# Performance work log

Measured on AMD Instinct MI355X. Metric: run time of the kernel, lower is better.

## Reference

```python
import jax, jax.numpy as jnp
import numpy as np

MARGIN = 0.2
MAX_VIOLATION = False
REDUCTION = 'mean'

N, D = 8192, 512


def setup_inputs() -> dict:
    key = jax.random.key(0)
    k1, k2, k3 = jax.random.split(key, 3)
    im = jax.random.normal(k1, (N, D), dtype=jnp.float32)
    s = jax.random.normal(k2, (N, D), dtype=jnp.float32)
    ex_s = jax.random.normal(k3, (N, D), dtype=jnp.float32)
    return {"im": im, "s": s, "ex_s": ex_s}


def l2_sim(im, s):
    # scores[i, j] = -||im_i - s_j||_2, computed via the GEMM identity
    # ||a-b||^2 = ||a||^2 + ||b||^2 - 2 a.b (same math, no NxNxD intermediate)
    im_sq = jnp.sum(im * im, axis=1)            # [N_im]
    s_sq = jnp.sum(s * s, axis=1)               # [N_s]
    d2 = im_sq[:, None] + s_sq[None, :] - 2.0 * (im @ s.T)  # [N_im, N_s]
    return -jnp.sqrt(jnp.maximum(d2, 0.0))


def reference(im, s, ex_s):
    scores = l2_sim(im, ex_s)        # [N_im, N_ex]
    scores_orig = l2_sim(im, s)      # [N_im, N_im]
    diagonal = jnp.diagonal(scores_orig)[:, None]            # [N_im, 1]
    cost_s = jnp.maximum(MARGIN + scores - diagonal, 0.0)    # [N_im, N_ex]
    if MAX_VIOLATION:
        cost_s = jnp.max(cost_s, axis=1)
    if REDUCTION == 'mean':
        return jnp.mean(cost_s)
    return jnp.sum(cost_s)
```

## Files before the change

kernel.cpp:

```cpp
#include <hip/hip_runtime.h>
#include <hip/hip_bf16.h>

#define NROW 8192
#define DDIM 512
#define MARGIN 0.2f

typedef __bf16 bf16x8 __attribute__((ext_vector_type(8)));
typedef float f32x4 __attribute__((ext_vector_type(4)));

__device__ __forceinline__ void gload16(const void* g, void* l) {
    __builtin_amdgcn_global_load_lds(
        (const __attribute__((address_space(1))) void*)g,
        (__attribute__((address_space(3))) void*)l, 16, 0, 0);
}

#define BAR() __builtin_amdgcn_s_barrier()

__global__ __launch_bounds__(256) void prep_kernel(
    const float* __restrict__ im, const float* __restrict__ s,
    const float* __restrict__ ex,
    ushort* __restrict__ Abf, ushort* __restrict__ Bbf,
    float2* __restrict__ idat, float* __restrict__ exsq) {
    int b = blockIdx.x;
    bool isim = b < NROW;
    int row = isim ? b : b - NROW;
    const float* src = isim ? im : ex;
    ushort* dst = isim ? Abf : Bbf;
    int tid = threadIdx.x;

    float2 v = ((const float2*)(src + (size_t)row * DDIM))[tid];
    __hip_bfloat16 hx = __float2bfloat16(v.x);
    __hip_bfloat16 hy = __float2bfloat16(v.y);
    unsigned packed = (unsigned)*(const ushort*)&hx | ((unsigned)*(const ushort*)&hy << 16);
    ((unsigned*)(dst + (size_t)row * DDIM))[tid] = packed;

    float ssq = v.x * v.x + v.y * v.y;
    float dsq = 0.f;
    if (isim) {
        float2 sv = ((const float2*)(s + (size_t)row * DDIM))[tid];
        float dx = v.x - sv.x, dy = v.y - sv.y;
        dsq = dx * dx + dy * dy;
    }
    #pragma unroll
    for (int off = 32; off > 0; off >>= 1) {
        ssq += __shfl_down(ssq, off);
        dsq += __shfl_down(dsq, off);
    }
    __shared__ float sred[8];
    int lane = tid & 63, w = tid >> 6;
    if (lane == 0) { sred[w] = ssq; sred[4 + w] = dsq; }
    __syncthreads();
    if (tid == 0) {
        float S = sred[0] + sred[1] + sred[2] + sred[3];
        float Dd = sred[4] + sred[5] + sred[6] + sred[7];
        if (isim) idat[row] = make_float2(S, MARGIN + sqrtf(Dd));
        else      exsq[row] = S;
    }
}

__global__ __launch_bounds__(256, 2) void gemm_cost_kernel(
    const ushort* __restrict__ Abf, const ushort* __restrict__ Bbf,
    const float2* __restrict__ idat, const float* __restrict__ exsq,
    float* __restrict__ partials) {
    __shared__ __align__(16) ushort sA[2][8192];
    __shared__ __align__(16) ushort sB[2][8192];
    __shared__ float redbuf[4];

    int bid0 = blockIdx.x;
    int c = bid0 & 7;
    int sq = bid0 >> 3;
    int win = sq >> 6;
    int pos = sq & 63;
    int bi = c * 8 + (pos & 7);
    int bj = win * 8 + (pos >> 3);
    int bid = bi * 64 + bj;
    int ibase = bi * 128, jbase = bj * 128;
    int tid = threadIdx.x, lane = tid & 63, w = tid >> 6;
    int wr = w >> 1, wc = w & 1;

    int r = tid >> 3;
    int pc = tid & 7;
    int lc = pc ^ (r & 7);
    const ushort* aG = Abf + (size_t)(ibase + r) * DDIM + lc * 8;
    const ushort* bG = Bbf + (size_t)(jbase + r) * DDIM + lc * 8;
    ushort* aL = &sA[0][0] + r * 64 + pc * 8;
    ushort* bL = &sB[0][0] + r * 64 + pc * 8;

    auto STAGE = [&](int h) {
        if (h >= 32) return;
        int kt = h >> 2, q = h & 3;
        if (q < 2) {
            const ushort* g = aG + q * (64 * DDIM) + kt * 64;
            ushort* l = aL + (kt & 1) * 8192 + q * 4096;
            gload16(g, l);
            gload16(g + 32 * DDIM, l + 2048);
        } else {
            int qq = q - 2;
            const ushort* g = bG + qq * (64 * DDIM) + kt * 64;
            ushort* l = bL + (kt & 1) * 8192 + qq * 4096;
            gload16(g, l);
            gload16(g + 32 * DDIM, l + 2048);
        }
    };

    int l15 = lane & 15;
    int pc0 = (((lane >> 4) ^ (lane & 7)) * 8);
    int pc1 = pc0 ^ 32;
    int aoff = (wr * 64 + l15) * 64;
    int boff = (wc * 64 + l15) * 64;

    f32x4 acc[4][4] = {};

    STAGE(0); STAGE(1); STAGE(2); STAGE(3);
    STAGE(4); STAGE(5); STAGE(6); STAGE(7);
    asm volatile("s_waitcnt vmcnt(8)" ::: "memory");
    BAR();

    #pragma unroll
    for (int t = 0; t < 8; ++t) {
        const ushort* pA = &sA[t & 1][0];
        const ushort* pB = &sB[t & 1][0];
        bf16x8 a[4][2], b[4][2];

        #pragma unroll
        for (int m = 0; m < 4; ++m) {
            a[m][0] = *(const bf16x8*)(pA + aoff + m * 1024 + pc0);
            a[m][1] = *(const bf16x8*)(pA + aoff + m * 1024 + pc1);
        }
        #pragma unroll
        for (int n = 0; n < 4; ++n) {
            b[n][0] = *(const bf16x8*)(pB + boff + n * 1024 + pc0);
            b[n][1] = *(const bf16x8*)(pB + boff + n * 1024 + pc1);
        }
        __builtin_amdgcn_s_setprio(1);
        #pragma unroll
        for (int m = 0; m < 4; ++m)
            #pragma unroll
            for (int n = 0; n < 4; ++n) {
                acc[m][n] = __builtin_amdgcn_mfma_f32_16x16x32_bf16(a[m][0], b[n][0], acc[m][n], 0, 0, 0);
                acc[m][n] = __builtin_amdgcn_mfma_f32_16x16x32_bf16(a[m][1], b[n][1], acc[m][n], 0, 0, 0);
            }
        __builtin_amdgcn_s_setprio(0);

        BAR();
        STAGE(4 * (t + 2) + 0); STAGE(4 * (t + 2) + 1);
        STAGE(4 * (t + 2) + 2); STAGE(4 * (t + 2) + 3);
        if (t < 6)       asm volatile("s_waitcnt vmcnt(8)" ::: "memory");
        else if (t == 6) asm volatile("s_waitcnt vmcnt(0)" ::: "memory");
        BAR();
    }

    float jt[4];
    #pragma unroll
    for (int n = 0; n < 4; ++n) jt[n] = exsq[jbase + wc * 64 + n * 16 + l15];
    int r0 = (lane >> 4) * 4;
    float lsum = 0.f;
    #pragma unroll
    for (int m = 0; m < 4; ++m) {
        #pragma unroll
        for (int rg = 0; rg < 4; ++rg) {
            int i = ibase + wr * 64 + m * 16 + r0 + rg;
            float2 id = idat[i];
            #pragma unroll
            for (int n = 0; n < 4; ++n) {
                float d2 = fmaxf(id.x + jt[n] - 2.0f * acc[m][n][rg], 0.0f);
                lsum += fmaxf(id.y - sqrtf(d2), 0.0f);
            }
        }
    }
    #pragma unroll
    for (int off = 32; off > 0; off >>= 1) lsum += __shfl_down(lsum, off);
    if (lane == 0) redbuf[w] = lsum;
    __syncthreads();
    if (tid == 0) partials[bid] = redbuf[0] + redbuf[1] + redbuf[2] + redbuf[3];
}

__global__ __launch_bounds__(256) void finalize_kernel(
    const float* __restrict__ partials, float* __restrict__ out) {
    float acc = 0.f;
    for (int t = threadIdx.x; t < 4096; t += 256) acc += partials[t];
    #pragma unroll
    for (int off = 32; off > 0; off >>= 1) acc += __shfl_down(acc, off);
    __shared__ float sred[4];
    int lane = threadIdx.x & 63, w = threadIdx.x >> 6;
    if (lane == 0) sred[w] = acc;
    __syncthreads();
    if (threadIdx.x == 0) {
        float total = sred[0] + sred[1] + sred[2] + sred[3];
        out[0] = total * (1.0f / (8192.0f * 8192.0f));
    }
}

extern "C" void kernel_launch(void* const* d_in, const int* in_sizes, int n_in,
                              void* d_out, int out_size, void* d_ws, size_t ws_size,
                              hipStream_t stream) {
    const float* im = (const float*)d_in[0];
    const float* s  = (const float*)d_in[1];
    const float* ex = (const float*)d_in[2];

    char* ws = (char*)d_ws;
    ushort* Abf   = (ushort*)(ws);
    ushort* Bbf   = (ushort*)(ws + 8388608);
    float2* idat  = (float2*)(ws + 16777216);
    float*  exsq  = (float*)(ws + 16842752);
    float*  parts = (float*)(ws + 16875520);

    prep_kernel<<<2 * NROW, 256, 0, stream>>>(im, s, ex, Abf, Bbf, idat, exsq);
    gemm_cost_kernel<<<(NROW / 128) * (NROW / 128), 256, 0, stream>>>(Abf, Bbf, idat, exsq, parts);
    finalize_kernel<<<1, 256, 0, stream>>>(parts, (float*)d_out);
}
```

Measured before the change: 111.4 us.

## Load B operand directly from global into registers, bypassing LDS

Removes the shared-memory staging buffer for the B (ex_s) tile. Each wave now reads its MFMA B fragments straight from global memory into double-buffered registers, prefetching the next k-step after the current MFMAs. This halves LDS usage and removes the LDS reads for B. In exchange it adds vector registers, duplicates B loads across the two wave rows that share a column, and uses narrower, less coalesced global accesses whose latency is waited on inside each iteration.

```diff
diff --git a/kernel.cpp b/kernel.cpp
--- a/kernel.cpp
+++ b/kernel.cpp
@@ -63,7 +63,6 @@
     const float2* __restrict__ idat, const float* __restrict__ exsq,
     float* __restrict__ partials) {
     __shared__ __align__(16) ushort sA[2][8192];
-    __shared__ __align__(16) ushort sB[2][8192];
     __shared__ float redbuf[4];
 
     int bid0 = blockIdx.x;
@@ -82,71 +81,72 @@
     int pc = tid & 7;
     int lc = pc ^ (r & 7);
     const ushort* aG = Abf + (size_t)(ibase + r) * DDIM + lc * 8;
-    const ushort* bG = Bbf + (size_t)(jbase + r) * DDIM + lc * 8;
     ushort* aL = &sA[0][0] + r * 64 + pc * 8;
-    ushort* bL = &sB[0][0] + r * 64 + pc * 8;
 
     auto STAGE = [&](int h) {
-        if (h >= 32) return;
-        int kt = h >> 2, q = h & 3;
-        if (q < 2) {
-            const ushort* g = aG + q * (64 * DDIM) + kt * 64;
-            ushort* l = aL + (kt & 1) * 8192 + q * 4096;
-            gload16(g, l);
-            gload16(g + 32 * DDIM, l + 2048);
-        } else {
-            int qq = q - 2;
-            const ushort* g = bG + qq * (64 * DDIM) + kt * 64;
-            ushort* l = bL + (kt & 1) * 8192 + qq * 4096;
-            gload16(g, l);
-            gload16(g + 32 * DDIM, l + 2048);
-        }
+        if (h >= 16) return;
+        int kt = h >> 1, q = h & 1;
+        const ushort* g = aG + q * (64 * DDIM) + kt * 64;
+        ushort* l = aL + (kt & 1) * 8192 + q * 4096;
+        gload16(g, l);
+        gload16(g + 32 * DDIM, l + 2048);
     };
 
     int l15 = lane & 15;
     int pc0 = (((lane >> 4) ^ (lane & 7)) * 8);
     int pc1 = pc0 ^ 32;
     int aoff = (wr * 64 + l15) * 64;
-    int boff = (wc * 64 + l15) * 64;
+
+    const ushort* bG = Bbf + (size_t)(jbase + wc * 64 + l15) * DDIM + (lane >> 4) * 8;
+
+    bf16x8 bA[4][2], bB[4][2];
+    auto LOADB = [&](int t, bf16x8 (&b)[4][2]) {
+        if (t >= 8) return;
+        #pragma unroll
+        for (int n = 0; n < 4; ++n)
+            #pragma unroll
+            for (int ks = 0; ks < 2; ++ks)
+                b[n][ks] = *(const bf16x8*)(bG + (size_t)n * 16 * DDIM + t * 64 + ks * 32);
+    };
 
     f32x4 acc[4][4] = {};
 
-    STAGE(0); STAGE(1); STAGE(2); STAGE(3);
-    STAGE(4); STAGE(5); STAGE(6); STAGE(7);
-    asm volatile("s_waitcnt vmcnt(8)" ::: "memory");
+    STAGE(0); STAGE(1);
+    LOADB(0, bA);
+    STAGE(2); STAGE(3);
+    asm volatile("s_waitcnt vmcnt(4)" ::: "memory");
+    __builtin_amdgcn_sched_barrier(0);
     BAR();
 
     #pragma unroll
     for (int t = 0; t < 8; ++t) {
         const ushort* pA = &sA[t & 1][0];
-        const ushort* pB = &sB[t & 1][0];
-        bf16x8 a[4][2], b[4][2];
+        bf16x8 (&bcur)[4][2] = (t & 1) ? bB : bA;
+        bf16x8 (&bnxt)[4][2] = (t & 1) ? bA : bB;
+        bf16x8 a[4][2];
 
         #pragma unroll
         for (int m = 0; m < 4; ++m) {
             a[m][0] = *(const bf16x8*)(pA + aoff + m * 1024 + pc0);
             a[m][1] = *(const bf16x8*)(pA + aoff + m * 1024 + pc1);
         }
-        #pragma unroll
-        for (int n = 0; n < 4; ++n) {
-            b[n][0] = *(const bf16x8*)(pB + boff + n * 1024 + pc0);
-            b[n][1] = *(const bf16x8*)(pB + boff + n * 1024 + pc1);
-        }
         __builtin_amdgcn_s_setprio(1);
         #pragma unroll
         for (int m = 0; m < 4; ++m)
             #pragma unroll
             for (int n = 0; n < 4; ++n) {
-                acc[m][n] = __builtin_amdgcn_mfma_f32_16x16x32_bf16(a[m][0], b[n][0], acc[m][n], 0, 0, 0);
-                acc[m][n] = __builtin_amdgcn_mfma_f32_16x16x32_bf16(a[m][1], b[n][1], acc[m][n], 0, 0, 0);
+                acc[m][n] = __builtin_amdgcn_mfma_f32_16x16x32_bf16(a[m][0], bcur[n][0], acc[m][n], 0, 0, 0);
+                acc[m][n] = __builtin_amdgcn_mfma_f32_16x16x32_bf16(a[m][1], bcur[n][1], acc[m][n], 0, 0, 0);
             }
         __builtin_amdgcn_s_setprio(0);
+        LOADB(t + 1, bnxt);
 
         BAR();
-        STAGE(4 * (t + 2) + 0); STAGE(4 * (t + 2) + 1);
-        STAGE(4 * (t + 2) + 2); STAGE(4 * (t + 2) + 3);
-        if (t < 6)       asm volatile("s_waitcnt vmcnt(8)" ::: "memory");
+        STAGE(2 * (t + 2));
+        STAGE(2 * (t + 2) + 1);
+        if (t < 6)       asm volatile("s_waitcnt vmcnt(4)" ::: "memory");
         else if (t == 6) asm volatile("s_waitcnt vmcnt(0)" ::: "memory");
+        __builtin_amdgcn_sched_barrier(0);
         BAR();
     }
 
```

Result: slower. 189.7 us (+70.2%).

## Triple-buffer LDS stages and prefetch next-tile fragments into registers

Applied to the files above, without the earlier changes.

The GEMM mainloop moves from a double-buffered LDS ring to a three-stage ring that holds A and B together, so global loads are issued two k-tiles ahead. It also double-buffers the register fragments: LDS reads for the next k-tile are issued before the current tile's MFMAs, so LDS latency can hide behind matrix math. The larger LDS footprint (about 96KB) and extra registers force launch bounds down to one block per SIMD group, which lowers occupancy and the latency hiding that comes from running other blocks.

```diff
diff --git a/kernel.cpp b/kernel.cpp
--- a/kernel.cpp
+++ b/kernel.cpp
@@ -58,12 +58,11 @@
     }
 }
 
-__global__ __launch_bounds__(256, 2) void gemm_cost_kernel(
+__global__ __launch_bounds__(256, 1) void gemm_cost_kernel(
     const ushort* __restrict__ Abf, const ushort* __restrict__ Bbf,
     const float2* __restrict__ idat, const float* __restrict__ exsq,
     float* __restrict__ partials) {
-    __shared__ __align__(16) ushort sA[2][8192];
-    __shared__ __align__(16) ushort sB[2][8192];
+    __shared__ __align__(16) ushort sAB[3][16384];
     __shared__ float redbuf[4];
 
     int bid0 = blockIdx.x;
@@ -83,70 +82,84 @@
     int lc = pc ^ (r & 7);
     const ushort* aG = Abf + (size_t)(ibase + r) * DDIM + lc * 8;
     const ushort* bG = Bbf + (size_t)(jbase + r) * DDIM + lc * 8;
-    ushort* aL = &sA[0][0] + r * 64 + pc * 8;
-    ushort* bL = &sB[0][0] + r * 64 + pc * 8;
-
-    auto STAGE = [&](int h) {
-        if (h >= 32) return;
-        int kt = h >> 2, q = h & 3;
-        if (q < 2) {
-            const ushort* g = aG + q * (64 * DDIM) + kt * 64;
-            ushort* l = aL + (kt & 1) * 8192 + q * 4096;
-            gload16(g, l);
-            gload16(g + 32 * DDIM, l + 2048);
-        } else {
-            int qq = q - 2;
-            const ushort* g = bG + qq * (64 * DDIM) + kt * 64;
-            ushort* l = bL + (kt & 1) * 8192 + qq * 4096;
-            gload16(g, l);
-            gload16(g + 32 * DDIM, l + 2048);
-        }
+    ushort* lL = &sAB[0][0] + r * 64 + pc * 8;
+
+    auto STAGE = [&](int kt) {
+        if (kt >= 8) return;
+        ushort* base = lL + (kt % 3) * 16384;
+        const ushort* ga = aG + kt * 64;
+        const ushort* gb = bG + kt * 64;
+        #pragma unroll
+        for (int q = 0; q < 4; ++q)
+            gload16(ga + q * (32 * DDIM), base + q * 2048);
+        #pragma unroll
+        for (int q = 0; q < 4; ++q)
+            gload16(gb + q * (32 * DDIM), base + 8192 + q * 2048);
     };
 
     int l15 = lane & 15;
     int pc0 = (((lane >> 4) ^ (lane & 7)) * 8);
     int pc1 = pc0 ^ 32;
     int aoff = (wr * 64 + l15) * 64;
-    int boff = (wc * 64 + l15) * 64;
+    int boff = 8192 + (wc * 64 + l15) * 64;
 
     f32x4 acc[4][4] = {};
-
-    STAGE(0); STAGE(1); STAGE(2); STAGE(3);
-    STAGE(4); STAGE(5); STAGE(6); STAGE(7);
+    bf16x8 aR0[4][2], aR1[4][2], bR0[4][2], bR1[4][2];
+
+    STAGE(0); STAGE(1); STAGE(2);
     asm volatile("s_waitcnt vmcnt(8)" ::: "memory");
+    __builtin_amdgcn_sched_barrier(0);
     BAR();
+    {
+        const ushort* p0 = &sAB[0][0];
+        #pragma unroll
+        for (int m = 0; m < 4; ++m) {
+            aR0[m][0] = *(const bf16x8*)(p0 + aoff + m * 1024 + pc0);
+            aR0[m][1] = *(const bf16x8*)(p0 + aoff + m * 1024 + pc1);
+        }
+        #pragma unroll
+        for (int n = 0; n < 4; ++n) {
+            bR0[n][0] = *(const bf16x8*)(p0 + boff + n * 1024 + pc0);
+            bR0[n][1] = *(const bf16x8*)(p0 + boff + n * 1024 + pc1);
+        }
+    }
 
     #pragma unroll
     for (int t = 0; t < 8; ++t) {
-        const ushort* pA = &sA[t & 1][0];
-        const ushort* pB = &sB[t & 1][0];
-        bf16x8 a[4][2], b[4][2];
-
-        #pragma unroll
-        for (int m = 0; m < 4; ++m) {
-            a[m][0] = *(const bf16x8*)(pA + aoff + m * 1024 + pc0);
-            a[m][1] = *(const bf16x8*)(pA + aoff + m * 1024 + pc1);
-        }
-        #pragma unroll
-        for (int n = 0; n < 4; ++n) {
-            b[n][0] = *(const bf16x8*)(pB + boff + n * 1024 + pc0);
-            b[n][1] = *(const bf16x8*)(pB + boff + n * 1024 + pc1);
-        }
+        bf16x8 (&ac)[4][2] = (t & 1) ? aR1 : aR0;
+        bf16x8 (&bc)[4][2] = (t & 1) ? bR1 : bR0;
+        bf16x8 (&an)[4][2] = (t & 1) ? aR0 : aR1;
+        bf16x8 (&bn)[4][2] = (t & 1) ? bR0 : bR1;
+
+        if (t < 7) {
+            const ushort* pN = &sAB[0][0] + ((t + 1) % 3) * 16384;
+            #pragma unroll
+            for (int m = 0; m < 4; ++m) {
+                an[m][0] = *(const bf16x8*)(pN + aoff + m * 1024 + pc0);
+                an[m][1] = *(const bf16x8*)(pN + aoff + m * 1024 + pc1);
+            }
+            #pragma unroll
+            for (int n = 0; n < 4; ++n) {
+                bn[n][0] = *(const bf16x8*)(pN + boff + n * 1024 + pc0);
+                bn[n][1] = *(const bf16x8*)(pN + boff + n * 1024 + pc1);
+            }
+        }
+
         __builtin_amdgcn_s_setprio(1);
         #pragma unroll
         for (int m = 0; m < 4; ++m)
             #pragma unroll
             for (int n = 0; n < 4; ++n) {
-                acc[m][n] = __builtin_amdgcn_mfma_f32_16x16x32_bf16(a[m][0], b[n][0], acc[m][n], 0, 0, 0);
-                acc[m][n] = __builtin_amdgcn_mfma_f32_16x16x32_bf16(a[m][1], b[n][1], acc[m][n], 0, 0, 0);
+                acc[m][n] = __builtin_amdgcn_mfma_f32_16x16x32_bf16(ac[m][0], bc[n][0], acc[m][n], 0, 0, 0);
+                acc[m][n] = __builtin_amdgcn_mfma_f32_16x16x32_bf16(ac[m][1], bc[n][1], acc[m][n], 0, 0, 0);
             }
         __builtin_amdgcn_s_setprio(0);
 
         BAR();
-        STAGE(4 * (t + 2) + 0); STAGE(4 * (t + 2) + 1);
-        STAGE(4 * (t + 2) + 2); STAGE(4 * (t + 2) + 3);
-        if (t < 6)       asm volatile("s_waitcnt vmcnt(8)" ::: "memory");
-        else if (t == 6) asm volatile("s_waitcnt vmcnt(0)" ::: "memory");
+        STAGE(t + 3);
+        if (t < 5)       asm volatile("s_waitcnt vmcnt(8)" ::: "memory");
+        else if (t == 5) asm volatile("s_waitcnt vmcnt(0)" ::: "memory");
+        __builtin_amdgcn_sched_barrier(0);
         BAR();
     }
 
```

Result: slower. 169.9 us (+52.5%).
